# Optimization experiments

Measured on AMD Instinct MI355X. Metric: run time of the kernel, lower is better.

The kernel has to match this reference:

```python
import jax, jax.numpy as jnp
import numpy as np

B, L, D = 4, 2048, 1024
DK, H = 64, 16
DFF = 4 * D
MASK_FILL = -2**15 + 1  # -32767, matches masked_fill value in source


def setup_inputs() -> dict:
    key = jax.random.key(0)
    ks = jax.random.split(key, 16)
    s = lambda fan_in: 1.0 / np.sqrt(fan_in)
    inp = {
        "x": jax.random.normal(ks[0], (B, L, D), dtype=jnp.float32),
        "maskPAD": jax.random.randint(ks[1], (B, L, L), 0, 2, dtype=jnp.int32),
        # attention projections (torch Linear layout: [out, in])
        "WQ_w": jax.random.uniform(ks[2], (H * DK, D), jnp.float32, -s(D), s(D)),
        "WQ_b": jnp.zeros((H * DK,), jnp.float32),
        "WK_w": jax.random.uniform(ks[3], (H * DK, D), jnp.float32, -s(D), s(D)),
        "WK_b": jnp.zeros((H * DK,), jnp.float32),
        "WV_w": jax.random.uniform(ks[4], (H * DK, D), jnp.float32, -s(D), s(D)),
        "WV_b": jnp.zeros((H * DK,), jnp.float32),
        "WO_w": jax.random.uniform(ks[5], (D, H * DK), jnp.float32, -s(H * DK), s(H * DK)),
        "WO_b": jnp.zeros((D,), jnp.float32),
        # FFN (pre-LN inside the FFN block)
        "ln_g": jnp.ones((D,), jnp.float32),
        "ln_b": jnp.zeros((D,), jnp.float32),
        "W1_w": jax.random.uniform(ks[6], (DFF, D), jnp.float32, -s(D), s(D)),
        "W1_b": jnp.zeros((DFF,), jnp.float32),
        "W2_w": jax.random.uniform(ks[7], (D, DFF), jnp.float32, -s(DFF), s(DFF)),
        "W2_b": jnp.zeros((D,), jnp.float32),
    }
    return inp


def _layernorm(x, g, b, eps=1e-5):
    mu = jnp.mean(x, axis=-1, keepdims=True)
    var = jnp.var(x, axis=-1, keepdims=True)
    return (x - mu) * jax.lax.rsqrt(var + eps) * g + b


def reference(x, maskPAD, WQ_w, WQ_b, WK_w, WK_b, WV_w, WV_b, WO_w, WO_b,
              ln_g, ln_b, W1_w, W1_b, W2_w, W2_b):
    # --- SelfAttention_PostLN (dropout = identity at eval) ---
    q = (jnp.einsum('bld,ed->ble', x, WQ_w) + WQ_b).reshape(B, L, H, DK).transpose(0, 2, 1, 3)
    k = (jnp.einsum('bld,ed->ble', x, WK_w) + WK_b).reshape(B, L, H, DK).transpose(0, 2, 1, 3)
    v = (jnp.einsum('bld,ed->ble', x, WV_w) + WV_b).reshape(B, L, H, DK).transpose(0, 2, 1, 3)
    scores = jnp.einsum('bhqd,bhkd->bhqk', q, k) / np.sqrt(DK).astype(np.float32)
    scores = jnp.where((maskPAD == 0)[:, None, :, :], jnp.float32(MASK_FILL), scores)
    alpha = jax.nn.softmax(scores, axis=-1)
    z = jnp.einsum('bhqk,bhkd->bhqd', alpha, v)  # [B,H,L,DK]
    z = z.transpose(0, 2, 1, 3).reshape(B, L, H * DK)
    z = jnp.einsum('ble,de->bld', z, WO_w) + WO_b
    # --- FFN_PreLN ---
    r = x + z                                    # residual 1 (dropout identity)
    h = _layernorm(r, ln_g, ln_b)
    h = jax.nn.relu(jnp.einsum('bld,fd->blf', h, W1_w) + W1_b)
    h = jnp.einsum('blf,df->bld', h, W2_w) + W2_b
    return r + h
```

## Files before the change

kernel.cpp:

```cpp
#include <hip/hip_runtime.h>

#define BD      4
#define LSEQ    2048
#define DMODEL  1024
#define HHEADS  16
#define DKK     64
#define DFFN    4096
#define MROWS   (BD*LSEQ)
#define QKS     2048

typedef float  f32x4  __attribute__((ext_vector_type(4)));
typedef float  f32x16 __attribute__((ext_vector_type(16)));
typedef __bf16 bf16x8 __attribute__((ext_vector_type(8)));
typedef unsigned short u16x8 __attribute__((ext_vector_type(8)));
typedef unsigned int   u32x4 __attribute__((ext_vector_type(4)));

__device__ inline unsigned short f2bf(float x) {
    union { float f; unsigned u; } c; c.f = x;
    unsigned r = c.u + 0x7FFFu + ((c.u >> 16) & 1u);
    return (unsigned short)(r >> 16);
}

__global__ void cast_bf16_k(const float* __restrict__ in,
                            unsigned short* __restrict__ out, long n) {
    long i = ((long)blockIdx.x * blockDim.x + threadIdx.x) * 4;
    long stride = (long)gridDim.x * blockDim.x * 4;
    for (; i < n; i += stride) {
        float4 v = *(const float4*)(in + i);
        ushort4 o;
        o.x = f2bf(v.x); o.y = f2bf(v.y); o.z = f2bf(v.z); o.w = f2bf(v.w);
        *(ushort4*)(out + i) = o;
    }
}

__global__ void cast_weights_k(const float* __restrict__ wq, const float* __restrict__ wk,
                               const float* __restrict__ wv, const float* __restrict__ wo,
                               const float* __restrict__ w1, const float* __restrict__ w2,
                               unsigned short* __restrict__ dqkv, unsigned short* __restrict__ dwo,
                               unsigned short* __restrict__ dw1, unsigned short* __restrict__ dw2) {
    const long M1 = 1024*1024;
    long i = ((long)blockIdx.x * blockDim.x + threadIdx.x) * 4;
    long stride = (long)gridDim.x * blockDim.x * 4;
    for (; i < 12*M1; i += stride) {
        const float* src; unsigned short* dst;
        if      (i <   M1) { src = wq + i;          dst = dqkv + i; }
        else if (i < 2*M1) { src = wk + (i-M1);     dst = dqkv + i; }
        else if (i < 3*M1) { src = wv + (i-2*M1);   dst = dqkv + i; }
        else if (i < 4*M1) { src = wo + (i-3*M1);   dst = dwo + (i-3*M1); }
        else if (i < 8*M1) { src = w1 + (i-4*M1);   dst = dw1 + (i-4*M1); }
        else               { src = w2 + (i-8*M1);   dst = dw2 + (i-8*M1); }
        float4 v = *(const float4*)src;
        ushort4 o;
        o.x = f2bf(v.x); o.y = f2bf(v.y); o.z = f2bf(v.z); o.w = f2bf(v.w);
        *(ushort4*)dst = o;
    }
}

__global__ void concat3_k(const float* __restrict__ a, const float* __restrict__ b,
                          const float* __restrict__ c, float* __restrict__ o) {
    int i = blockIdx.x * 256 + threadIdx.x;
    if (i < 1024) { o[i] = a[i]; o[1024 + i] = b[i]; o[2048 + i] = c[i]; }
}

__global__ __launch_bounds__(256) void maskbits_k(const int* __restrict__ m,
                                                  unsigned long long* __restrict__ bits) {
    const long gw = ((long)blockIdx.x * blockDim.x + threadIdx.x) >> 6;
    const int lane = threadIdx.x & 63;
    const int b   = (int)(gw >> 16);
    const int rem = (int)gw & 65535;
    const int q = rem >> 5, kt = rem & 31;
    const int v = m[((size_t)(b*LSEQ + q))*LSEQ + kt*64 + lane];
    const unsigned long long bal = __ballot(v != 0);
    if (lane == 0) bits[((size_t)(b*32 + kt))*LSEQ + q] = bal;
}

__device__ inline void gload16(const void* g, void* l) {
    __builtin_amdgcn_global_load_lds(
        (const __attribute__((address_space(1))) void*)g,
        (__attribute__((address_space(3))) void*)l, 16, 0, 0);
}

#define BAR() { __builtin_amdgcn_sched_barrier(0); __builtin_amdgcn_s_barrier(); __builtin_amdgcn_sched_barrier(0); }

#define STAGE(XSEL, XPTR, h, tau, s)                                              \
  { const unsigned short* gs0 = (XPTR) + (size_t)((h)*128 + wid*8 + srow) * K + (tau)*64 + schk*8; \
    gload16(gs0, (void*)&sm[(s)][(XSEL)][(((h)*128 + wid*8)*64)]);                 \
    gload16(gs0 + (size_t)64*K, (void*)&sm[(s)][(XSEL)][(((h)*128 + 64 + wid*8)*64)]); }

#define LDA(dst, s, mi, kk) dst = *(const bf16x8*)(&sm[(s)][0][(wr*128 + (mi)*16 + r0)*64 + ((((kk)*4 + g) ^ (r0 & 7)) << 3)]);
#define LDB(dst, s, nj, kk) dst = *(const bf16x8*)(&sm[(s)][1][(wc*64  + (nj)*16 + r0)*64 + ((((kk)*4 + g) ^ (r0 & 7)) << 3)]);

#define PHASE_MFMA(q)                                                                                   \
    __builtin_amdgcn_s_setprio(1);                                                                      \
    _Pragma("unroll")                                                                                   \
    for (int nj = 0; nj < 4; ++nj) {                                                                    \
        acc[2*(q)][nj]   = __builtin_amdgcn_mfma_f32_16x16x32_bf16(af00, bq[nj][0], acc[2*(q)][nj],   0,0,0); \
        acc[2*(q)][nj]   = __builtin_amdgcn_mfma_f32_16x16x32_bf16(af01, bq[nj][1], acc[2*(q)][nj],   0,0,0); \
        acc[2*(q)+1][nj] = __builtin_amdgcn_mfma_f32_16x16x32_bf16(af10, bq[nj][0], acc[2*(q)+1][nj], 0,0,0); \
        acc[2*(q)+1][nj] = __builtin_amdgcn_mfma_f32_16x16x32_bf16(af11, bq[nj][1], acc[2*(q)+1][nj], 0,0,0); \
    }                                                                                                   \
    __builtin_amdgcn_s_setprio(0);

#define KTILE(s, tau)                                                        \
  {                                                                          \
    const int tp1 = (tau) + 1, tp2 = (tau) + 2;                              \
    bf16x8 bq[4][2];                                                         \
    bf16x8 af00, af01, af10, af11;                                           \
    _Pragma("unroll") for (int nj = 0; nj < 4; ++nj) {                       \
        LDB(bq[nj][0], s, nj, 0); LDB(bq[nj][1], s, nj, 1); }                \
    LDA(af00, s, 0, 0); LDA(af01, s, 0, 1);                                  \
    LDA(af10, s, 1, 0); LDA(af11, s, 1, 1);                                  \
    if (tp1 < NTT) { STAGE(0, Ab, 0, tp1, (s)^1); }                          \
    BAR(); PHASE_MFMA(0); BAR();                                             \
    LDA(af00, s, 2, 0); LDA(af01, s, 2, 1);                                  \
    LDA(af10, s, 3, 0); LDA(af11, s, 3, 1);                                  \
    if (tp1 < NTT) { STAGE(0, Ab, 1, tp1, (s)^1); }                          \
    if (tp2 < NTT) { STAGE(1, Bb, 0, tp2, (s)); }                            \
    BAR(); PHASE_MFMA(1); BAR();                                             \
    LDA(af00, s, 4, 0); LDA(af01, s, 4, 1);                                  \
    LDA(af10, s, 5, 0); LDA(af11, s, 5, 1);                                  \
    if (tp2 < NTT) { STAGE(1, Bb, 1, tp2, (s)); }                            \
    BAR(); PHASE_MFMA(2); BAR();                                             \
    LDA(af00, s, 6, 0); LDA(af01, s, 6, 1);                                  \
    LDA(af10, s, 7, 0); LDA(af11, s, 7, 1);                                  \
    if (tp2 < NTT)      { asm volatile("s_waitcnt vmcnt(4)" ::: "memory"); } \
    else if (tp1 < NTT) { asm volatile("s_waitcnt vmcnt(0)" ::: "memory"); } \
    BAR(); PHASE_MFMA(3); BAR();                                             \
  }

template<int MODE, int NTT>
__global__ __launch_bounds__(512, 1) void gemm8(const unsigned short* __restrict__ A,
                                                const unsigned short* __restrict__ B,
                                                const float* __restrict__ bias,
                                                const float* __restrict__ resid,
                                                void* __restrict__ Cout,
                                                unsigned short* __restrict__ vt,
                                                int M, int N, int K, float scaleQ)
{
    __shared__ unsigned short sm[2][2][256*64];
    const int t   = threadIdx.x;
    const int wid = t >> 6, lane = t & 63;
    const int wr  = wid >> 2, wc = wid & 3;
    const int r0  = lane & 15, g = lane >> 4;

    const int nwg = gridDim.x;
    const int bid = (blockIdx.x & 7) * (nwg >> 3) + (blockIdx.x >> 3);
    const int ntn = N >> 8;
    const int bm  = (bid / ntn) << 8, bn = (bid % ntn) << 8;

    const int srow = lane >> 3;
    const int schk = (lane & 7) ^ srow;
    const unsigned short* Ab = A + (size_t)bm * K;
    const unsigned short* Bb = B + (size_t)bn * K;

    f32x4 acc[8][4] = {};

    STAGE(1, Bb, 0, 0, 0); STAGE(1, Bb, 1, 0, 0);
    STAGE(0, Ab, 0, 0, 0); STAGE(0, Ab, 1, 0, 0);
    STAGE(1, Bb, 0, 1, 1); STAGE(1, Bb, 1, 1, 1);
    asm volatile("s_waitcnt vmcnt(4)" ::: "memory");
    BAR();

#pragma unroll 1
    for (int i2 = 0; i2 < NTT/2; ++i2) {
        const int tau = 2*i2;
        KTILE(0, tau);
        KTILE(1, tau+1);
    }

#pragma unroll
    for (int mi = 0; mi < 8; ++mi) {
        const int row0 = bm + wr*128 + mi*16 + g*4;
#pragma unroll
        for (int nj = 0; nj < 4; ++nj) {
            const int col = bn + wc*64 + nj*16 + r0;
            const float bcol = bias[col];
            if (MODE == 1) {
#pragma unroll
                for (int rr = 0; rr < 4; ++rr) {
                    float c = fmaxf(acc[mi][nj][rr] + bcol, 0.f);
                    ((unsigned short*)Cout)[(size_t)(row0 + rr) * N + col] = f2bf(c);
                }
            } else if (MODE == 2) {
#pragma unroll
                for (int rr = 0; rr < 4; ++rr) {
                    const size_t idx = (size_t)(row0 + rr) * N + col;
                    ((float*)Cout)[idx] = acc[mi][nj][rr] + bcol + resid[idx];
                }
            } else if (MODE == 3) {
                if (col < 2048) {
                    const float sc = (col < 1024) ? scaleQ : 1.0f;
#pragma unroll
                    for (int rr = 0; rr < 4; ++rr)
                        ((unsigned short*)Cout)[(size_t)(row0 + rr) * QKS + col] =
                            f2bf((acc[mi][nj][rr] + bcol) * sc);
                } else {
                    const int vcol = col - 2048;
                    const int b = row0 >> 11, tok = row0 & 2047;
                    ushort4 h4;
                    h4.x = f2bf(acc[mi][nj][0] + bcol);
                    h4.y = f2bf(acc[mi][nj][1] + bcol);
                    h4.z = f2bf(acc[mi][nj][2] + bcol);
                    h4.w = f2bf(acc[mi][nj][3] + bcol);
                    *(ushort4*)&vt[((size_t)(b*1024 + vcol))*LSEQ + tok] = h4;
                }
            }
        }
    }
}

#define STAGEA2(h, tau, s)                                                        \
  { const unsigned short* gs0 = Ab + (size_t)((h)*128 + wid*8 + srow) * K + (tau)*64 + schk*8; \
    gload16(gs0, (void*)&smA[(s)][(((h)*128 + wid*8)*64)]);                        \
    gload16(gs0 + (size_t)64*K, (void*)&smA[(s)][(((h)*128 + 64 + wid*8)*64)]); }

#define STAGEB2(tau, s)                                                           \
  { const unsigned short* gs0 = Bb + (size_t)(wid*8 + srow) * K + (tau)*64 + schk*8; \
    gload16(gs0, (void*)&smB[(s)][((wid*8)*64)]);                                  \
    gload16(gs0 + (size_t)64*K, (void*)&smB[(s)][((64 + wid*8)*64)]); }

#define LDA2(dst, s, mi, kk) dst = *(const bf16x8*)(&smA[(s)][(wr*128 + (mi)*16 + r0)*64 + ((((kk)*4 + g) ^ (r0 & 7)) << 3)]);
#define LDB2(dst, s, nj, kk) dst = *(const bf16x8*)(&smB[(s)][(wc*32  + (nj)*16 + r0)*64 + ((((kk)*4 + g) ^ (r0 & 7)) << 3)]);

#define PHASE_MFMA2X(q0)                                                                                \
    __builtin_amdgcn_s_setprio(1);                                                                      \
    _Pragma("unroll")                                                                                   \
    for (int mm = 0; mm < 4; ++mm) {                                                                    \
        acc[(q0)+mm][0] = __builtin_amdgcn_mfma_f32_16x16x32_bf16(aa[2*mm],   bq[0][0], acc[(q0)+mm][0], 0,0,0); \
        acc[(q0)+mm][0] = __builtin_amdgcn_mfma_f32_16x16x32_bf16(aa[2*mm+1], bq[0][1], acc[(q0)+mm][0], 0,0,0); \
        acc[(q0)+mm][1] = __builtin_amdgcn_mfma_f32_16x16x32_bf16(aa[2*mm],   bq[1][0], acc[(q0)+mm][1], 0,0,0); \
        acc[(q0)+mm][1] = __builtin_amdgcn_mfma_f32_16x16x32_bf16(aa[2*mm+1], bq[1][1], acc[(q0)+mm][1], 0,0,0); \
    }                                                                                                   \
    __builtin_amdgcn_s_setprio(0);

#define KTILE2(s, tau)                                                       \
  {                                                                          \
    const int tp1 = (tau) + 1, tp2 = (tau) + 2;                              \
    bf16x8 bq[2][2];                                                         \
    bf16x8 aa[8];                                                            \
    LDB2(bq[0][0], s, 0, 0); LDB2(bq[0][1], s, 0, 1);                        \
    LDB2(bq[1][0], s, 1, 0); LDB2(bq[1][1], s, 1, 1);                        \
    LDA2(aa[0], s, 0, 0); LDA2(aa[1], s, 0, 1);                              \
    LDA2(aa[2], s, 1, 0); LDA2(aa[3], s, 1, 1);                              \
    LDA2(aa[4], s, 2, 0); LDA2(aa[5], s, 2, 1);                              \
    LDA2(aa[6], s, 3, 0); LDA2(aa[7], s, 3, 1);                              \
    if (tp1 < NTT) { STAGEA2(0, tp1, (s)^1); }                               \
    BAR(); PHASE_MFMA2X(0); BAR();                                           \
    LDA2(aa[0], s, 4, 0); LDA2(aa[1], s, 4, 1);                              \
    LDA2(aa[2], s, 5, 0); LDA2(aa[3], s, 5, 1);                              \
    LDA2(aa[4], s, 6, 0); LDA2(aa[5], s, 6, 1);                              \
    LDA2(aa[6], s, 7, 0); LDA2(aa[7], s, 7, 1);                              \
    if (tp1 < NTT) { STAGEA2(1, tp1, (s)^1); }                               \
    if (tp2 < NTT) { STAGEB2(tp2, (s)); }                                    \
    if (tp2 < NTT)      { asm volatile("s_waitcnt vmcnt(2)" ::: "memory"); } \
    else if (tp1 < NTT) { asm volatile("s_waitcnt vmcnt(0)" ::: "memory"); } \
    BAR(); PHASE_MFMA2X(4); BAR();                                           \
  }

template<int MODE, int NTT>
__global__ __launch_bounds__(512, 1) void gemm8n(const unsigned short* __restrict__ A,
                                                 const unsigned short* __restrict__ B,
                                                 const float* __restrict__ bias,
                                                 const float* __restrict__ resid,
                                                 void* __restrict__ Cout,
                                                 int M, int N, int K)
{
    __shared__ unsigned short smA[2][256*64];
    __shared__ unsigned short smB[2][128*64];
    const int t   = threadIdx.x;
    const int wid = t >> 6, lane = t & 63;
    const int wr  = wid >> 2, wc = wid & 3;
    const int r0  = lane & 15, g = lane >> 4;

    const int nwg = gridDim.x;
    const int bid = (blockIdx.x & 7) * (nwg >> 3) + (blockIdx.x >> 3);
    const int ntn = N >> 7;
    const int bm  = (bid / ntn) << 8, bn = (bid % ntn) << 7;

    const int srow = lane >> 3;
    const int schk = (lane & 7) ^ srow;
    const unsigned short* Ab = A + (size_t)bm * K;
    const unsigned short* Bb = B + (size_t)bn * K;

    f32x4 acc[8][2] = {};

    STAGEB2(0, 0);
    STAGEA2(0, 0, 0); STAGEA2(1, 0, 0);
    STAGEB2(1, 1);
    asm volatile("s_waitcnt vmcnt(2)" ::: "memory");
    BAR();

#pragma unroll 1
    for (int i2 = 0; i2 < NTT/2; ++i2) {
        const int tau = 2*i2;
        KTILE2(0, tau);
        KTILE2(1, tau+1);
    }

#pragma unroll
    for (int mi = 0; mi < 8; ++mi) {
        const int row0 = bm + wr*128 + mi*16 + g*4;
#pragma unroll
        for (int nj = 0; nj < 2; ++nj) {
            const int col = bn + wc*32 + nj*16 + r0;
            const float bcol = bias[col];
#pragma unroll
            for (int rr = 0; rr < 4; ++rr) {
                const int row = row0 + rr;
                if (MODE == 2) {
                    float c = acc[mi][nj][rr] + bcol;
                    ((float*)Cout)[(size_t)row * N + col] = c + resid[(size_t)row * N + col];
                }
            }
        }
    }
}

#define MFILL   (-47272.79f)
#define DEFTHR  (11.5415603f)
__global__ __launch_bounds__(256, 3) void attn_k(
    const unsigned short* __restrict__ QK,
    const unsigned short* __restrict__ VT,
    const unsigned long long* __restrict__ MBits,
    unsigned short* __restrict__ Z)
{
    __shared__ unsigned short Ks[2][64*64];
    __shared__ unsigned short Vs[2][64*64];
    __shared__ float Sc[4*32];

    const int t    = threadIdx.x;
    const int w    = t >> 6, lane = t & 63;
    const int q31  = lane & 31, hi = lane >> 5;

    const int bid = blockIdx.x;
    const int sw  = (bid & 7) * 128 + (bid >> 3);
    const int qt  = sw & 15, h = (sw >> 4) & 15, b = sw >> 8;
    const int qw  = qt * 128 + w * 32;

    const unsigned short* Qg = QK + ((size_t)(b*LSEQ + qw + q31))*QKS + h*DKK + hi*8;
    bf16x8 qf[4];
#pragma unroll
    for (int ds = 0; ds < 4; ++ds)
        qf[ds] = *(const bf16x8*)(Qg + ds*16);

    const int srow = w*8 + (lane>>3);
    const int schk = (lane & 7) ^ (srow & 7);
    const unsigned short* kP = QK + ((size_t)(b*LSEQ))*QKS + 1024 + h*DKK
                                  + (size_t)srow*QKS + schk*8;
    const unsigned short* vP = VT + ((size_t)(b*1024 + h*DKK))*LSEQ
                                  + (size_t)srow*LSEQ + schk*8;
    const unsigned long long* mP = MBits + ((size_t)(b*32))*LSEQ + (qw + q31);

    float m_r = MFILL, l_r = 0.f;
    f32x16 z0, z1;
#pragma unroll
    for (int r = 0; r < 16; ++r) { z0[r] = 0.f; z1[r] = 0.f; }

    gload16(kP,           &Ks[0][w*512]);
    gload16(kP + 32*QKS,  &Ks[0][w*512] + 2048);
    gload16(vP,           &Vs[0][w*512]);
    gload16(vP + 32*LSEQ, &Vs[0][w*512] + 2048);
    unsigned long long mw = *mP;
    kP += 64*QKS; vP += 64; mP += LSEQ;

    for (int kt = 0; kt < LSEQ/64; ++kt) {
        const int cur = kt & 1;
        __syncthreads();

        gload16(kP,           &Ks[cur^1][w*512]);
        gload16(kP + 32*QKS,  &Ks[cur^1][w*512] + 2048);
        gload16(vP,           &Vs[cur^1][w*512]);
        gload16(vP + 32*LSEQ, &Vs[cur^1][w*512] + 2048);
        const unsigned long long mwn = (kt < LSEQ/64 - 1) ? *mP : mw;
        kP += 64*QKS; vP += 64; mP += LSEQ;

        const unsigned long long sh = mw >> (hi*4);
        const unsigned md0 = (unsigned)sh, md1 = (unsigned)(sh >> 32);

        f32x16 s0, s1;
#pragma unroll
        for (int r = 0; r < 16; ++r) { s0[r] = 0.f; s1[r] = 0.f; }
        __builtin_amdgcn_s_setprio(1);
#pragma unroll
        for (int ds = 0; ds < 4; ++ds) {
            const int slot = ((ds*2 + hi) ^ (q31 & 7)) << 3;
            bf16x8 kf0 = *(const bf16x8*)(&Ks[cur][ q31     *64 + slot]);
            bf16x8 kf1 = *(const bf16x8*)(&Ks[cur][(32+q31)*64 + slot]);
            s0 = __builtin_amdgcn_mfma_f32_32x32x16_bf16(kf0, qf[ds], s0, 0, 0, 0);
            s1 = __builtin_amdgcn_mfma_f32_32x32x16_bf16(kf1, qf[ds], s1, 0, 0, 0);
        }
        __builtin_amdgcn_s_setprio(0);

        float a8[16];
#pragma unroll
        for (int r = 0; r < 16; ++r) a8[r] = fmaxf(s0[r], s1[r]);
        {
            float t0 = fmaxf(fmaxf(a8[0],  a8[1]),  a8[2]);
            float t1 = fmaxf(fmaxf(a8[3],  a8[4]),  a8[5]);
            float t2 = fmaxf(fmaxf(a8[6],  a8[7]),  a8[8]);
            float t3 = fmaxf(fmaxf(a8[9],  a8[10]), a8[11]);
            float t4 = fmaxf(fmaxf(a8[12], a8[13]), a8[14]);
            float u0 = fmaxf(fmaxf(t0, t1), t2);
            float u1 = fmaxf(fmaxf(t3, t4), a8[15]);
            float tm = fmaxf(u0, u1);
            float ta = tm, tb = tm;
            asm volatile("v_permlane32_swap_b32 %0, %1" : "+v"(ta), "+v"(tb));
            tm = fmaxf(tm, hi ? ta : tb);

            if (__any(tm > m_r + DEFTHR)) {
                const float nm   = fmaxf(m_r, tm);
                const float corr = exp2f(m_r - nm);
                Sc[w*32 + q31] = corr;
                l_r *= corr;
                m_r  = nm;
#pragma unroll
                for (int r = 0; r < 16; ++r) {
                    const int row = (r & 3) + 8*(r >> 2) + 4*hi;
                    const float cr = Sc[w*32 + row];
                    z0[r] *= cr; z1[r] *= cr;
                }
            }
        }

#pragma unroll
        for (int r = 0; r < 16; ++r) {
            const int kb = (r & 3) + 8*(r >> 2);
            s0[r] = exp2f(s0[r] - m_r);
            s1[r] = exp2f(s1[r] - m_r);
            if (!((md0 >> kb) & 1)) s0[r] = 0.f;
            if (!((md1 >> kb) & 1)) s1[r] = 0.f;
        }
        float r4[8];
#pragma unroll
        for (int r = 0; r < 8; ++r)
            r4[r] = (s0[2*r] + s0[2*r+1]) + (s1[2*r] + s1[2*r+1]);
        float rs = ((r4[0]+r4[1]) + (r4[2]+r4[3])) + ((r4[4]+r4[5]) + (r4[6]+r4[7]));
        {
            float ra = rs, rb = rs;
            asm volatile("v_permlane32_swap_b32 %0, %1" : "+v"(ra), "+v"(rb));
            rs += hi ? ra : rb;
        }
        l_r += rs;

        __builtin_amdgcn_s_setprio(1);
#pragma unroll
        for (int half = 0; half < 2; ++half) {
#pragma unroll
            for (int sub = 0; sub < 2; ++sub) {
                const int base = sub*8;
                unsigned wa, wb, wc2, wd;
                float p0 = half ? s1[base+0] : s0[base+0];
                float p1 = half ? s1[base+1] : s0[base+1];
                float p2 = half ? s1[base+2] : s0[base+2];
                float p3 = half ? s1[base+3] : s0[base+3];
                float p4 = half ? s1[base+4] : s0[base+4];
                float p5 = half ? s1[base+5] : s0[base+5];
                float p6 = half ? s1[base+6] : s0[base+6];
                float p7 = half ? s1[base+7] : s0[base+7];
                asm("v_cvt_pk_bf16_f32 %0, %1, %2" : "=v"(wa) : "v"(p0), "v"(p1));
                asm("v_cvt_pk_bf16_f32 %0, %1, %2" : "=v"(wb) : "v"(p4), "v"(p5));
                asm("v_cvt_pk_bf16_f32 %0, %1, %2" : "=v"(wc2) : "v"(p2), "v"(p3));
                asm("v_cvt_pk_bf16_f32 %0, %1, %2" : "=v"(wd) : "v"(p6), "v"(p7));
                asm volatile("v_permlane32_swap_b32 %0, %1" : "+v"(wa), "+v"(wb));
                asm volatile("v_permlane32_swap_b32 %0, %1" : "+v"(wc2), "+v"(wd));
                u32x4 pu; pu[0] = wa; pu[1] = wc2; pu[2] = wb; pu[3] = wd;
                bf16x8 pa = __builtin_bit_cast(bf16x8, pu);
                const int ks = half*2 + sub;
                const int slot = ((ks*2 + hi) ^ (q31 & 7)) << 3;
                bf16x8 vf0 = *(const bf16x8*)(&Vs[cur][ q31     *64 + slot]);
                bf16x8 vf1 = *(const bf16x8*)(&Vs[cur][(32+q31)*64 + slot]);
                z0 = __builtin_amdgcn_mfma_f32_32x32x16_bf16(pa, vf0, z0, 0, 0, 0);
                z1 = __builtin_amdgcn_mfma_f32_32x32x16_bf16(pa, vf1, z1, 0, 0, 0);
            }
        }
        __builtin_amdgcn_s_setprio(0);

        mw = mwn;
    }

    Sc[w*32 + q31] = l_r;
    unsigned short* Zb = Z + ((size_t)(b*LSEQ + qw))*DMODEL + h*DKK + q31;
#pragma unroll
    for (int r = 0; r < 16; ++r) {
        const int row = (r & 3) + 8*(r >> 2) + 4*hi;
        const float rl = 1.0f / Sc[w*32 + row];
        Zb[(size_t)row*DMODEL]      = f2bf(z0[r] * rl);
        Zb[(size_t)row*DMODEL + 32] = f2bf(z1[r] * rl);
    }
}

__global__ __launch_bounds__(256) void ln_k(const float* __restrict__ r,
                                            const float* __restrict__ gam,
                                            const float* __restrict__ bet,
                                            unsigned short* __restrict__ out)
{
    const int row = blockIdx.x;
    const int t = threadIdx.x;
    const float* rp = r + (size_t)row * DMODEL;
    float4 v = *(const float4*)(rp + t*4);
    float s  = v.x + v.y + v.z + v.w;
    float s2 = v.x*v.x + v.y*v.y + v.z*v.z + v.w*v.w;
#pragma unroll
    for (int off = 32; off >= 1; off >>= 1) {
        s  += __shfl_xor(s,  off);
        s2 += __shfl_xor(s2, off);
    }
    __shared__ float red[8];
    const int wv = t >> 6;
    if ((t & 63) == 0) { red[wv] = s; red[4 + wv] = s2; }
    __syncthreads();
    s  = red[0] + red[1] + red[2] + red[3];
    s2 = red[4] + red[5] + red[6] + red[7];
    const float mu   = s  * (1.f/DMODEL);
    const float var  = s2 * (1.f/DMODEL) - mu*mu;
    const float rstd = rsqrtf(var + 1e-5f);
    float4 gv = *(const float4*)(gam + t*4);
    float4 bv = *(const float4*)(bet + t*4);
    ushort4 o;
    o.x = f2bf((v.x - mu)*rstd*gv.x + bv.x);
    o.y = f2bf((v.y - mu)*rstd*gv.y + bv.y);
    o.z = f2bf((v.z - mu)*rstd*gv.z + bv.z);
    o.w = f2bf((v.w - mu)*rstd*gv.w + bv.w);
    *(ushort4*)(out + (size_t)row * DMODEL + t*4) = o;
}

extern "C" void kernel_launch(void* const* d_in, const int* in_sizes, int n_in,
                              void* d_out, int out_size, void* d_ws, size_t ws_size,
                              hipStream_t stream)
{
    const float* x    = (const float*)d_in[0];
    const int*   mask = (const int*)  d_in[1];
    const float* WQ_w = (const float*)d_in[2];
    const float* WQ_b = (const float*)d_in[3];
    const float* WK_w = (const float*)d_in[4];
    const float* WK_b = (const float*)d_in[5];
    const float* WV_w = (const float*)d_in[6];
    const float* WV_b = (const float*)d_in[7];
    const float* WO_w = (const float*)d_in[8];
    const float* WO_b = (const float*)d_in[9];
    const float* ln_g = (const float*)d_in[10];
    const float* ln_b = (const float*)d_in[11];
    const float* W1_w = (const float*)d_in[12];
    const float* W1_b = (const float*)d_in[13];
    const float* W2_w = (const float*)d_in[14];
    const float* W2_b = (const float*)d_in[15];
    float* out = (float*)d_out;

    char* w = (char*)d_ws;
    const size_t MB = 1024*1024;
    unsigned short* qk   = (unsigned short*)(w + 0*MB);
    unsigned short* vtb  = (unsigned short*)(w + 32*MB);
    unsigned short* shr  = (unsigned short*)(w + 64*MB);
    float*          rb   = (float*)         (w + 80*MB);
    unsigned short* wqkv = (unsigned short*)(w + 112*MB);
    unsigned short* wob  = (unsigned short*)(w + 118*MB);
    unsigned short* w1b  = (unsigned short*)(w + 120*MB);
    unsigned short* w2b  = (unsigned short*)(w + 128*MB);
    unsigned long long* mbits = (unsigned long long*)(w + 136*MB);
    float* bqkv = (float*)rb;
    unsigned short* xb   = shr;
    unsigned short* Zb   = shr;
    unsigned short* hln  = shr;
    unsigned short* hmid = (unsigned short*)(w + 0*MB);

    cast_bf16_k<<<2048, 256, 0, stream>>>(x, xb, (long)MROWS*DMODEL);
    cast_weights_k<<<2048, 256, 0, stream>>>(WQ_w, WK_w, WV_w, WO_w, W1_w, W2_w,
                                             wqkv, wob, w1b, w2b);
    maskbits_k<<<65536, 256, 0, stream>>>(mask, mbits);
    concat3_k<<<4, 256, 0, stream>>>(WQ_b, WK_b, WV_b, bqkv);

    gemm8<3, 16><<<dim3(384), dim3(512), 0, stream>>>(xb, wqkv, bqkv, nullptr, qk, vtb,
                                                      MROWS, 3072, DMODEL, 0.18033688f);
    attn_k<<<dim3(1024), dim3(256), 0, stream>>>(qk, vtb, mbits, Zb);
    gemm8n<2, 16><<<dim3(256), dim3(512), 0, stream>>>(Zb, wob, WO_b, x, rb,
                                                       MROWS, DMODEL, DMODEL);
    ln_k<<<MROWS, 256, 0, stream>>>(rb, ln_g, ln_b, hln);
    gemm8<1, 16><<<dim3(512), dim3(512), 0, stream>>>(hln, w1b, W1_b, nullptr, hmid, nullptr,
                                                      MROWS, DFFN, DMODEL, 1.0f);
    gemm8<2, 64><<<dim3(128), dim3(512), 0, stream>>>(hmid, w2b, W2_b, rb, out, nullptr,
                                                      MROWS, DMODEL, DFFN, 1.0f);
}
```

Measured before the change: 474.3 us.

## Split-K the FFN down-projection with bf16 partials and a separate reduce kernel

The final FFN GEMM (K=4096) used to launch only 128 workgroups, which leaves many compute units idle. It now splits K in half across 256 workgroups. Each half writes bf16 partial sums into reused workspace buffers, and a new elementwise kernel adds the two partials, the bias and the residual to produce the output. The QKV bias concatenation is also folded into the weight-cast kernel, which removes one launch. The cost is extra global memory traffic and a launch for the reduction, plus some precision loss from rounding partial sums to bf16.

Result: faster. 443.5 us (-6.5%).

```diff
diff --git a/kernel.cpp b/kernel.cpp
--- a/kernel.cpp
+++ b/kernel.cpp
@@ -19,6 +19,10 @@
     union { float f; unsigned u; } c; c.f = x;
     unsigned r = c.u + 0x7FFFu + ((c.u >> 16) & 1u);
     return (unsigned short)(r >> 16);
+}
+__device__ inline float bf2f(unsigned short u) {
+    union { unsigned u; float f; } c; c.u = ((unsigned)u) << 16;
+    return c.f;
 }
 
 __global__ void cast_bf16_k(const float* __restrict__ in,
@@ -37,7 +41,13 @@
                                const float* __restrict__ wv, const float* __restrict__ wo,
                                const float* __restrict__ w1, const float* __restrict__ w2,
                                unsigned short* __restrict__ dqkv, unsigned short* __restrict__ dwo,
-                               unsigned short* __restrict__ dw1, unsigned short* __restrict__ dw2) {
+                               unsigned short* __restrict__ dw1, unsigned short* __restrict__ dw2,
+                               const float* __restrict__ bq, const float* __restrict__ bk,
+                               const float* __restrict__ bv, float* __restrict__ bqkv) {
+    if (blockIdx.x < 4) {
+        int j = blockIdx.x * 256 + threadIdx.x;
+        if (j < 1024) { bqkv[j] = bq[j]; bqkv[1024 + j] = bk[j]; bqkv[2048 + j] = bv[j]; }
+    }
     const long M1 = 1024*1024;
     long i = ((long)blockIdx.x * blockDim.x + threadIdx.x) * 4;
     long stride = (long)gridDim.x * blockDim.x * 4;
@@ -56,12 +66,6 @@
     }
 }
 
-__global__ void concat3_k(const float* __restrict__ a, const float* __restrict__ b,
-                          const float* __restrict__ c, float* __restrict__ o) {
-    int i = blockIdx.x * 256 + threadIdx.x;
-    if (i < 1024) { o[i] = a[i]; o[1024 + i] = b[i]; o[2048 + i] = c[i]; }
-}
-
 __global__ __launch_bounds__(256) void maskbits_k(const int* __restrict__ m,
                                                   unsigned long long* __restrict__ bits) {
     const long gw = ((long)blockIdx.x * blockDim.x + threadIdx.x) >> 6;
@@ -72,6 +76,27 @@
     const int v = m[((size_t)(b*LSEQ + q))*LSEQ + kt*64 + lane];
     const unsigned long long bal = __ballot(v != 0);
     if (lane == 0) bits[((size_t)(b*32 + kt))*LSEQ + q] = bal;
+}
+
+__global__ void reduce2_k(const unsigned short* __restrict__ p0,
+                          const unsigned short* __restrict__ p1,
+                          const float* __restrict__ rb,
+                          const float* __restrict__ b2,
+                          float* __restrict__ out) {
+    long i = ((long)blockIdx.x * blockDim.x + threadIdx.x) * 4;
+    long stride = (long)gridDim.x * blockDim.x * 4;
+    for (; i < (long)MROWS*DMODEL; i += stride) {
+        ushort4 a = *(const ushort4*)(p0 + i);
+        ushort4 b = *(const ushort4*)(p1 + i);
+        float4 r  = *(const float4*)(rb + i);
+        float4 bias = *(const float4*)(b2 + (int)(i & (DMODEL-1)));
+        float4 o;
+        o.x = r.x + bias.x + bf2f(a.x) + bf2f(b.x);
+        o.y = r.y + bias.y + bf2f(a.y) + bf2f(b.y);
+        o.z = r.z + bias.z + bf2f(a.z) + bf2f(b.z);
+        o.w = r.w + bias.w + bf2f(a.w) + bf2f(b.w);
+        *(float4*)(out + i) = o;
+    }
 }
 
 __device__ inline void gload16(const void* g, void* l) {
@@ -145,13 +170,24 @@
 
     const int nwg = gridDim.x;
     const int bid = (blockIdx.x & 7) * (nwg >> 3) + (blockIdx.x >> 3);
-    const int ntn = N >> 8;
-    const int bm  = (bid / ntn) << 8, bn = (bid % ntn) << 8;
+
+    int bm, bn, koff = 0;
+    unsigned short* Pout = (unsigned short*)Cout;
+    if (MODE == 4) {
+        const int tile = bid >> 1, kh = bid & 1;
+        const int ntn = N >> 8;
+        bm = (tile / ntn) << 8; bn = (tile % ntn) << 8;
+        koff = kh * (K >> 1);
+        if (kh) Pout = vt;
+    } else {
+        const int ntn = N >> 8;
+        bm = (bid / ntn) << 8; bn = (bid % ntn) << 8;
+    }
 
     const int srow = lane >> 3;
     const int schk = (lane & 7) ^ srow;
-    const unsigned short* Ab = A + (size_t)bm * K;
-    const unsigned short* Bb = B + (size_t)bn * K;
+    const unsigned short* Ab = A + (size_t)bm * K + koff;
+    const unsigned short* Bb = B + (size_t)bn * K + koff;
 
     f32x4 acc[8][4] = {};
 
@@ -174,7 +210,7 @@
 #pragma unroll
         for (int nj = 0; nj < 4; ++nj) {
             const int col = bn + wc*64 + nj*16 + r0;
-            const float bcol = bias[col];
+            const float bcol = (MODE == 4) ? 0.f : bias[col];
             if (MODE == 1) {
 #pragma unroll
                 for (int rr = 0; rr < 4; ++rr) {
@@ -187,6 +223,10 @@
                     const size_t idx = (size_t)(row0 + rr) * N + col;
                     ((float*)Cout)[idx] = acc[mi][nj][rr] + bcol + resid[idx];
                 }
+            } else if (MODE == 4) {
+#pragma unroll
+                for (int rr = 0; rr < 4; ++rr)
+                    Pout[(size_t)(row0 + rr) * N + col] = f2bf(acc[mi][nj][rr]);
             } else if (MODE == 3) {
                 if (col < 2048) {
                     const float sc = (col < 1024) ? scaleQ : 1.0f;
@@ -562,12 +602,14 @@
     unsigned short* Zb   = shr;
     unsigned short* hln  = shr;
     unsigned short* hmid = (unsigned short*)(w + 0*MB);
+    unsigned short* P0   = shr;
+    unsigned short* P1   = wqkv;
 
     cast_bf16_k<<<2048, 256, 0, stream>>>(x, xb, (long)MROWS*DMODEL);
     cast_weights_k<<<2048, 256, 0, stream>>>(WQ_w, WK_w, WV_w, WO_w, W1_w, W2_w,
-                                             wqkv, wob, w1b, w2b);
+                                             wqkv, wob, w1b, w2b,
+                                             WQ_b, WK_b, WV_b, bqkv);
     maskbits_k<<<65536, 256, 0, stream>>>(mask, mbits);
-    concat3_k<<<4, 256, 0, stream>>>(WQ_b, WK_b, WV_b, bqkv);
 
     gemm8<3, 16><<<dim3(384), dim3(512), 0, stream>>>(xb, wqkv, bqkv, nullptr, qk, vtb,
                                                       MROWS, 3072, DMODEL, 0.18033688f);
@@ -577,6 +619,7 @@
     ln_k<<<MROWS, 256, 0, stream>>>(rb, ln_g, ln_b, hln);
     gemm8<1, 16><<<dim3(512), dim3(512), 0, stream>>>(hln, w1b, W1_b, nullptr, hmid, nullptr,
                                                       MROWS, DFFN, DMODEL, 1.0f);
-    gemm8<2, 64><<<dim3(128), dim3(512), 0, stream>>>(hmid, w2b, W2_b, rb, out, nullptr,
+    gemm8<4, 32><<<dim3(256), dim3(512), 0, stream>>>(hmid, w2b, nullptr, nullptr, P0, P1,
                                                       MROWS, DMODEL, DFFN, 1.0f);
-}
+    reduce2_k<<<2048, 256, 0, stream>>>(P0, P1, rb, W2_b, out);
+}
```
